# Kernel optimization log

Measured on AMD Instinct MI355X. Metric: run time of the kernel, lower is better.

Reference implementation:

```python
import jax, jax.numpy as jnp
import numpy as np

B, S, D = 2, 2048, 1024
H, DH, DL, DR = 16, 64, 512, 64
DHID, N_SHARED, N_ROUTED, TOPK = 512, 2, 8, 2
EPS = 1e-6


def setup_inputs() -> dict:
    key = jax.random.key(0)
    ks = jax.random.split(key, 16)
    w = lambda k, shp: jax.random.normal(k, shp, dtype=jnp.float32) * 0.02
    return {
        "x": jax.random.normal(ks[0], (B, S, D), dtype=jnp.float32),
        "mask": jnp.tril(jnp.ones((S, S), dtype=bool)),  # causal
        "w_q": w(ks[1], (D, H * (DH + DR))),
        "w_dkv": w(ks[2], (D, DL)),
        "w_uk": w(ks[3], (DL, H * DH)),
        "w_uv": w(ks[4], (DL, H * DH)),
        "w_kr": w(ks[5], (D, DR)),
        "w_o": w(ks[6], (H * DH, D)),
        "attn_norm_w": jnp.ones((D,), jnp.float32),
        "mlp_norm_w": jnp.ones((D,), jnp.float32),
        "gate_w": w(ks[7], (D, N_ROUTED)),
        "wr_gate": w(ks[8], (N_ROUTED, D, DHID)),
        "wr_up": w(ks[9], (N_ROUTED, D, DHID)),
        "wr_down": w(ks[10], (N_ROUTED, DHID, D)),
        "ws_gate": w(ks[11], (N_SHARED, D, DHID)),
        "ws_up": w(ks[12], (N_SHARED, D, DHID)),
        "ws_down": w(ks[13], (N_SHARED, DHID, D)),
    }


def _rmsnorm(x, w):
    x32 = x.astype(jnp.float32)
    n = x32 * jax.lax.rsqrt(jnp.mean(x32 * x32, axis=-1, keepdims=True) + EPS)
    return n.astype(x.dtype) * w


def _rope_tables(seq_len, dim):
    half = dim // 2
    inv = 1.0 / (10000.0 ** (jnp.arange(half, dtype=jnp.float32) / half))
    ang = jnp.arange(seq_len, dtype=jnp.float32)[:, None] * inv[None, :]  # [S, dim/2]
    return jnp.cos(ang), jnp.sin(ang)


def _rope(t, cos, sin):
    # t: [..., S, dim]; rotate-half convention
    t1, t2 = jnp.split(t, 2, axis=-1)
    return jnp.concatenate([t1 * cos - t2 * sin, t2 * cos + t1 * sin], axis=-1)


def _layer(x, mask, w_q, w_dkv, w_uk, w_uv, w_kr, w_o, attn_norm_w, mlp_norm_w,
           gate_w, wr_gate, wr_up, wr_down, ws_gate, ws_up, ws_down):
    # ---- pre-norm MLA attention + residual ----
    h = _rmsnorm(x, attn_norm_w)
    cos, sin = _rope_tables(S, DR)

    q = (h @ w_q).reshape(B, S, H, DH + DR).transpose(0, 2, 1, 3)  # [B,H,S,DH+DR]
    q_c, q_r = q[..., :DH], _rope(q[..., DH:], cos, sin)

    latent = h @ w_dkv                                              # [B,S,DL]
    k_c = (latent @ w_uk).reshape(B, S, H, DH).transpose(0, 2, 1, 3)  # [B,H,S,DH]
    v = (latent @ w_uv).reshape(B, S, H, DH).transpose(0, 2, 1, 3)
    k_r = _rope(h @ w_kr, cos, sin)                                 # [B,S,DR] shared across heads

    scale = 1.0 / np.sqrt(DH + DR)
    scores = (jnp.einsum("bhqd,bhkd->bhqk", q_c, k_c)
              + jnp.einsum("bhqd,bkd->bhqk", q_r, k_r)) * scale
    scores = jnp.where(mask, scores, jnp.float32(-1e9))
    attn = jax.nn.softmax(scores, axis=-1)
    ctx = jnp.einsum("bhqk,bhkd->bhqd", attn, v)                    # [B,H,S,DH]
    attn_out = ctx.transpose(0, 2, 1, 3).reshape(B, S, H * DH) @ w_o
    x = x + attn_out

    # ---- pre-norm shared + routed MoE FFN + residual ----
    h = _rmsnorm(x, mlp_norm_w).reshape(-1, D)                      # [T,D]
    probs = jax.nn.softmax(h @ gate_w, axis=-1)                     # [T,NR]
    vals, idx = jax.lax.top_k(probs, TOPK)                          # [T,K]
    gw = vals / jnp.sum(vals, axis=-1, keepdims=True)
    dense_w = jnp.sum(jax.nn.one_hot(idx, N_ROUTED, dtype=h.dtype) * gw[..., None], axis=1)  # [T,NR]

    g = jax.nn.silu(jnp.einsum("td,edh->teh", h, wr_gate))
    u = jnp.einsum("td,edh->teh", h, wr_up)
    y = jnp.einsum("teh,ehd->ted", g * u, wr_down)                  # [T,NR,D]
    routed = jnp.einsum("ted,te->td", y, dense_w)

    gs = jax.nn.silu(jnp.einsum("td,sdh->tsh", h, ws_gate))
    us = jnp.einsum("td,sdh->tsh", h, ws_up)
    shared = jnp.einsum("tsh,shd->td", gs * us, ws_down)

    return x + (routed + shared).reshape(B, S, D)


def reference(x, mask, w_q, w_dkv, w_uk, w_uv, w_kr, w_o, attn_norm_w, mlp_norm_w,
              gate_w, wr_gate, wr_up, wr_down, ws_gate, ws_up, ws_down):
    return _layer(x, mask, w_q, w_dkv, w_uk, w_uv, w_kr, w_o, attn_norm_w, mlp_norm_w,
                  gate_w, wr_gate, wr_up, wr_down, ws_gate, ws_up, ws_down)
```

## Files before the change

kernel.cpp:

```cpp
#include <hip/hip_runtime.h>
#include <hip/hip_bf16.h>
#include <stdint.h>

typedef unsigned short u16;
typedef __attribute__((ext_vector_type(8))) short short8;
typedef __attribute__((ext_vector_type(4))) float f32x4;
typedef __attribute__((ext_vector_type(4))) int i32x4;
typedef __attribute__((ext_vector_type(2))) unsigned int u32x2;

#define B_    2
#define S_    2048
#define D_    1024
#define H_    16
#define T_    (B_*S_)

static __device__ __forceinline__ float b2f(u16 h) { return __uint_as_float(((uint32_t)h) << 16); }
static __device__ __forceinline__ u16 f2b(float f) {
    uint32_t u = __float_as_uint(f);
    u += 0x7fffu + ((u >> 16) & 1u);
    return (u16)(u >> 16);
}
static __device__ __forceinline__ uint32_t pack2(float a, float b) {
    return (uint32_t)f2b(a) | ((uint32_t)f2b(b) << 16);
}
static __device__ __forceinline__ uint32_t cvtpk(float a, float b) {
    uint32_t r;
    asm("v_cvt_pk_bf16_f32 %0, %1, %2" : "=v"(r) : "v"(a), "v"(b));
    return r;
}
#define MFMA(a,b,c) __builtin_amdgcn_mfma_f32_16x16x32_bf16(a,b,c,0,0,0)

static __device__ __forceinline__ void gl2lds16(const void* g, void* l) {
    __builtin_amdgcn_global_load_lds((const __attribute__((address_space(1))) void*)g,
                                     (__attribute__((address_space(3))) void*)l, 16, 0, 0);
}

__global__ __launch_bounds__(256) void transpose_cvt(const float* __restrict__ in,
    u16* __restrict__ out, int K, int N, long inEZ, long outEZ)
{
    __shared__ float tile[32][33];
    const int e = blockIdx.z;
    const float* ip = in + (long)e * inEZ;
    u16* op = out + (long)e * outEZ;
    int n0 = blockIdx.x * 32, k0 = blockIdx.y * 32;
    int tx = threadIdx.x, ty = threadIdx.y;
#pragma unroll
    for (int i = 0; i < 4; ++i) {
        int k = k0 + ty + 8 * i, n = n0 + tx;
        tile[ty + 8 * i][tx] = (k < K && n < N) ? ip[(long)k * N + n] : 0.f;
    }
    __syncthreads();
#pragma unroll
    for (int i = 0; i < 4; ++i) {
        int n = n0 + ty + 8 * i, k = k0 + tx;
        if (n < N && k < K) op[(long)n * K + k] = f2b(tile[tx][ty + 8 * i]);
    }
}

__global__ __launch_bounds__(256) void gemm_k(const u16* __restrict__ A, long lda,
    const u16* __restrict__ Bt, long ldb, void* __restrict__ Cv, long ldc, int K,
    int mode, const float* __restrict__ resid)
{
    __shared__ u16 As[128 * 32];
    __shared__ u16 Bs[128 * 32];
    const int tid = threadIdx.x, lane = tid & 63, wave = tid >> 6;
    const int wm = (wave & 1) * 64, wn = (wave >> 1) * 64;
    const int quad = lane >> 4, rr = lane & 15, q8 = quad * 8;
    const long row0 = (long)blockIdx.y * 128, col0 = (long)blockIdx.x * 128;
    f32x4 acc[4][4];
#pragma unroll
    for (int i = 0; i < 4; ++i)
#pragma unroll
        for (int j = 0; j < 4; ++j)
#pragma unroll
            for (int c = 0; c < 4; ++c) acc[i][j][c] = 0.f;
    const int band = wave * 32;
    const u16* ga = A + (row0 + band + (lane >> 2)) * lda + (lane & 3) * 8;
    const u16* gb = Bt + (col0 + band + (lane >> 2)) * ldb + (lane & 3) * 8;
    u16* la = &As[band * 32];
    u16* lb = &Bs[band * 32];
    for (int k0 = 0; k0 < K; k0 += 32) {
        gl2lds16(ga + k0, la);
        gl2lds16(ga + k0 + 16 * lda, la + 16 * 32);
        gl2lds16(gb + k0, lb);
        gl2lds16(gb + k0 + 16 * ldb, lb + 16 * 32);
        __syncthreads();
        short8 af[4], bf[4];
#pragma unroll
        for (int mi = 0; mi < 4; ++mi) af[mi] = *(const short8*)&As[(wm + mi * 16 + rr) * 32 + q8];
#pragma unroll
        for (int ni = 0; ni < 4; ++ni) bf[ni] = *(const short8*)&Bs[(wn + ni * 16 + rr) * 32 + q8];
#pragma unroll
        for (int mi = 0; mi < 4; ++mi)
#pragma unroll
            for (int ni = 0; ni < 4; ++ni)
                acc[mi][ni] = MFMA(af[mi], bf[ni], acc[mi][ni]);
        __syncthreads();
    }
#pragma unroll
    for (int mi = 0; mi < 4; ++mi)
#pragma unroll
        for (int ni = 0; ni < 4; ++ni)
#pragma unroll
            for (int rg = 0; rg < 4; ++rg) {
                long r = row0 + wm + mi * 16 + quad * 4 + rg;
                long c = col0 + wn + ni * 16 + rr;
                float v = acc[mi][ni][rg];
                if (mode == 1)      ((u16*)Cv)[r * ldc + c] = f2b(v);
                else if (mode == 2) ((float*)Cv)[r * ldc + c] += v;
                else                ((float*)Cv)[r * ldc + c] = v + resid[r * 1024 + c];
            }
}

__global__ __launch_bounds__(256) void gemm_shdown(const u16* __restrict__ A,
    const u16* __restrict__ BtBase, float* __restrict__ Cv)
{
    __shared__ u16 As[128 * 32];
    __shared__ u16 Bs[128 * 32];
    const int tid = threadIdx.x, lane = tid & 63, wave = tid >> 6;
    const int wm = (wave & 1) * 64, wn = (wave >> 1) * 64;
    const int quad = lane >> 4, rr = lane & 15, q8 = quad * 8;
    const long row0 = (long)blockIdx.y * 128, col0 = (long)blockIdx.x * 128;
    f32x4 acc[4][4];
#pragma unroll
    for (int i = 0; i < 4; ++i)
#pragma unroll
        for (int j = 0; j < 4; ++j)
#pragma unroll
            for (int c = 0; c < 4; ++c) acc[i][j][c] = 0.f;
    const int band = wave * 32;
    const long arow = row0 + band + (lane >> 2);
    const long brow = col0 + band + (lane >> 2);
    u16* la = &As[band * 32];
    u16* lb = &Bs[band * 32];
    for (int k0 = 0; k0 < 1024; k0 += 32) {
        const long aoff = (k0 < 512) ? (long)k0 : (long)(512 + k0);
        const long boff = (k0 < 512) ? (long)k0 : (long)(524288 - 512 + k0);
        const u16* ga = A + arow * 2048 + aoff + (lane & 3) * 8;
        const u16* gb = BtBase + brow * 512 + boff + (lane & 3) * 8;
        gl2lds16(ga, la);
        gl2lds16(ga + 16 * 2048, la + 16 * 32);
        gl2lds16(gb, lb);
        gl2lds16(gb + 16 * 512, lb + 16 * 32);
        __syncthreads();
        short8 af[4], bf[4];
#pragma unroll
        for (int mi = 0; mi < 4; ++mi) af[mi] = *(const short8*)&As[(wm + mi * 16 + rr) * 32 + q8];
#pragma unroll
        for (int ni = 0; ni < 4; ++ni) bf[ni] = *(const short8*)&Bs[(wn + ni * 16 + rr) * 32 + q8];
#pragma unroll
        for (int mi = 0; mi < 4; ++mi)
#pragma unroll
            for (int ni = 0; ni < 4; ++ni)
                acc[mi][ni] = MFMA(af[mi], bf[ni], acc[mi][ni]);
        __syncthreads();
    }
#pragma unroll
    for (int mi = 0; mi < 4; ++mi)
#pragma unroll
        for (int ni = 0; ni < 4; ++ni)
#pragma unroll
            for (int rg = 0; rg < 4; ++rg) {
                long r = row0 + wm + mi * 16 + quad * 4 + rg;
                long c = col0 + wn + ni * 16 + rr;
                Cv[r * 1024 + c] += acc[mi][ni][rg];
            }
}

__global__ __launch_bounds__(256) void gemm_gather(const u16* __restrict__ H2,
    const u16* __restrict__ BtAll, u16* __restrict__ C,
    const int* __restrict__ cnt, const int* __restrict__ off,
    const int* __restrict__ elist)
{
    const int e = blockIdx.z;
    const int cntE = cnt[e], offE = off[e];
    const int m0 = blockIdx.y * 128;
    if (m0 >= cntE) return;
    const u16* Bt = BtAll + (long)e * 1024 * 1024;
    __shared__ u16 As[128 * 32];
    __shared__ u16 Bs[128 * 32];
    const int tid = threadIdx.x, lane = tid & 63, wave = tid >> 6;
    const int wm = (wave & 1) * 64, wn = (wave >> 1) * 64;
    const int quad = lane >> 4, rr = lane & 15, q8 = quad * 8;
    const long col0 = (long)blockIdx.x * 128;
    f32x4 acc[4][4];
#pragma unroll
    for (int i = 0; i < 4; ++i)
#pragma unroll
        for (int j = 0; j < 4; ++j)
#pragma unroll
            for (int c = 0; c < 4; ++c) acc[i][j][c] = 0.f;
    const int band = wave * 32;
    int r0 = m0 + band + (lane >> 2);
    int r1 = r0 + 16;
    int tok0 = elist[offE + (r0 < cntE ? r0 : cntE - 1)];
    int tok1 = elist[offE + (r1 < cntE ? r1 : cntE - 1)];
    const u16* ga0 = H2 + (long)tok0 * 1024 + (lane & 3) * 8;
    const u16* ga1 = H2 + (long)tok1 * 1024 + (lane & 3) * 8;
    const u16* gb = Bt + (col0 + band + (lane >> 2)) * 1024L + (lane & 3) * 8;
    u16* la = &As[band * 32];
    u16* lb = &Bs[band * 32];
    for (int k0 = 0; k0 < 1024; k0 += 32) {
        gl2lds16(ga0 + k0, la);
        gl2lds16(ga1 + k0, la + 16 * 32);
        gl2lds16(gb + k0, lb);
        gl2lds16(gb + k0 + 16 * 1024, lb + 16 * 32);
        __syncthreads();
        short8 af[4], bf[4];
#pragma unroll
        for (int mi = 0; mi < 4; ++mi) af[mi] = *(const short8*)&As[(wm + mi * 16 + rr) * 32 + q8];
#pragma unroll
        for (int ni = 0; ni < 4; ++ni) bf[ni] = *(const short8*)&Bs[(wn + ni * 16 + rr) * 32 + q8];
#pragma unroll
        for (int mi = 0; mi < 4; ++mi)
#pragma unroll
            for (int ni = 0; ni < 4; ++ni)
                acc[mi][ni] = MFMA(af[mi], bf[ni], acc[mi][ni]);
        __syncthreads();
    }
#pragma unroll
    for (int mi = 0; mi < 4; ++mi)
#pragma unroll
        for (int ni = 0; ni < 4; ++ni)
#pragma unroll
            for (int rg = 0; rg < 4; ++rg) {
                int ml = wm + mi * 16 + quad * 4 + rg;
                long c = col0 + wn + ni * 16 + rr;
                if (m0 + ml < cntE)
                    C[(long)(offE + m0 + ml) * 1024 + c] = f2b(acc[mi][ni][rg]);
            }
}

__global__ __launch_bounds__(256) void gemm_slot(const u16* __restrict__ Act,
    const u16* __restrict__ BtAll, u16* __restrict__ rout,
    const int* __restrict__ cnt, const int* __restrict__ off)
{
    const int e = blockIdx.z;
    const int cntE = cnt[e], offE = off[e];
    const int m0 = blockIdx.y * 128;
    if (m0 >= cntE) return;
    const u16* Bt = BtAll + (long)e * 1024 * 512;
    __shared__ u16 As[128 * 32];
    __shared__ u16 Bs[128 * 32];
    const int tid = threadIdx.x, lane = tid & 63, wave = tid >> 6;
    const int wm = (wave & 1) * 64, wn = (wave >> 1) * 64;
    const int quad = lane >> 4, rr = lane & 15, q8 = quad * 8;
    const long col0 = (long)blockIdx.x * 128;
    f32x4 acc[4][4];
#pragma unroll
    for (int i = 0; i < 4; ++i)
#pragma unroll
        for (int j = 0; j < 4; ++j)
#pragma unroll
            for (int c = 0; c < 4; ++c) acc[i][j][c] = 0.f;
    const int band = wave * 32;
    int r0 = offE + m0 + band + (lane >> 2); if (r0 > 8191) r0 = 8191;
    int r1 = r0 + 16; if (r1 > 8191) r1 = 8191;
    const u16* ga0 = Act + (long)r0 * 1024 + (lane & 3) * 8;
    const u16* ga1 = Act + (long)r1 * 1024 + (lane & 3) * 8;
    const u16* gb = Bt + (col0 + band + (lane >> 2)) * 512L + (lane & 3) * 8;
    u16* la = &As[band * 32];
    u16* lb = &Bs[band * 32];
    for (int k0 = 0; k0 < 512; k0 += 32) {
        gl2lds16(ga0 + k0, la);
        gl2lds16(ga1 + k0, la + 16 * 32);
        gl2lds16(gb + k0, lb);
        gl2lds16(gb + k0 + 16 * 512, lb + 16 * 32);
        __syncthreads();
        short8 af[4], bf[4];
#pragma unroll
        for (int mi = 0; mi < 4; ++mi) af[mi] = *(const short8*)&As[(wm + mi * 16 + rr) * 32 + q8];
#pragma unroll
        for (int ni = 0; ni < 4; ++ni) bf[ni] = *(const short8*)&Bs[(wn + ni * 16 + rr) * 32 + q8];
#pragma unroll
        for (int mi = 0; mi < 4; ++mi)
#pragma unroll
            for (int ni = 0; ni < 4; ++ni)
                acc[mi][ni] = MFMA(af[mi], bf[ni], acc[mi][ni]);
        __syncthreads();
    }
#pragma unroll
    for (int mi = 0; mi < 4; ++mi)
#pragma unroll
        for (int ni = 0; ni < 4; ++ni)
#pragma unroll
            for (int rg = 0; rg < 4; ++rg) {
                int ml = wm + mi * 16 + quad * 4 + rg;
                long c = col0 + wn + ni * 16 + rr;
                if (m0 + ml < cntE)
                    rout[(long)(offE + m0 + ml) * 1024 + c] = f2b(acc[mi][ni][rg]);
            }
}

__global__ __launch_bounds__(256) void rmsnorm_wave(const float* __restrict__ x,
    const float* __restrict__ w, u16* __restrict__ out)
{
    const int t = blockIdx.x * 4 + (threadIdx.x >> 6);
    const int lane = threadIdx.x & 63;
    const float* xp = x + (size_t)t * D_;
    f32x4 v[4];
    float s = 0.f;
#pragma unroll
    for (int i = 0; i < 4; ++i) {
        v[i] = *(const f32x4*)&xp[lane * 4 + i * 256];
#pragma unroll
        for (int j = 0; j < 4; ++j) s += v[i][j] * v[i][j];
    }
#pragma unroll
    for (int o = 32; o > 0; o >>= 1) s += __shfl_xor(s, o);
    const float inv = rsqrtf(s * (1.f / D_) + 1e-6f);
    u16* op = out + (size_t)t * D_;
#pragma unroll
    for (int i = 0; i < 4; ++i) {
        const int d = lane * 4 + i * 256;
        f32x4 wv = *(const f32x4*)&w[d];
        u32x2 pk;
        pk[0] = pack2(v[i][0] * inv * wv[0], v[i][1] * inv * wv[1]);
        pk[1] = pack2(v[i][2] * inv * wv[2], v[i][3] * inv * wv[3]);
        *(u32x2*)&op[d] = pk;
    }
}

__global__ __launch_bounds__(256) void rmsnorm_gate_fused(const float* __restrict__ xm,
    const float* __restrict__ nw, const float* __restrict__ gw, u16* __restrict__ h2,
    int* __restrict__ tok_e, float* __restrict__ tok_w)
{
    const int t = blockIdx.x * 4 + (threadIdx.x >> 6);
    const int lane = threadIdx.x & 63;
    const float* xp = xm + (size_t)t * D_;
    f32x4 v[4];
    float s = 0.f;
#pragma unroll
    for (int i = 0; i < 4; ++i) {
        v[i] = *(const f32x4*)&xp[lane * 4 + i * 256];
#pragma unroll
        for (int j = 0; j < 4; ++j) s += v[i][j] * v[i][j];
    }
#pragma unroll
    for (int o = 32; o > 0; o >>= 1) s += __shfl_xor(s, o);
    const float inv = rsqrtf(s * (1.f / D_) + 1e-6f);
    u16* op = h2 + (size_t)t * D_;
    float part[8] = {0,0,0,0,0,0,0,0};
#pragma unroll
    for (int i = 0; i < 4; ++i) {
        const int d = lane * 4 + i * 256;
        f32x4 wv = *(const f32x4*)&nw[d];
        float hv[4];
#pragma unroll
        for (int j = 0; j < 4; ++j) hv[j] = v[i][j] * inv * wv[j];
        u32x2 pk;
        pk[0] = pack2(hv[0], hv[1]);
        pk[1] = pack2(hv[2], hv[3]);
        *(u32x2*)&op[d] = pk;
#pragma unroll
        for (int j = 0; j < 4; ++j) {
            const float* gp = gw + (size_t)(d + j) * 8;
#pragma unroll
            for (int e = 0; e < 8; ++e) part[e] += hv[j] * gp[e];
        }
    }
#pragma unroll
    for (int e = 0; e < 8; ++e)
#pragma unroll
        for (int o = 32; o > 0; o >>= 1) part[e] += __shfl_xor(part[e], o);
    if (lane == 0) {
        float mx = part[0];
#pragma unroll
        for (int e = 1; e < 8; ++e) mx = fmaxf(mx, part[e]);
        float p[8];
#pragma unroll
        for (int e = 0; e < 8; ++e) p[e] = __expf(part[e] - mx);
        int i0 = 0;
#pragma unroll
        for (int e = 1; e < 8; ++e) if (p[e] > p[i0]) i0 = e;
        int i1 = (i0 == 0) ? 1 : 0;
#pragma unroll
        for (int e = 0; e < 8; ++e) { if (e == i0) continue; if (p[e] > p[i1]) i1 = e; }
        float sw = p[i0] + p[i1];
        tok_e[2 * t] = i0;  tok_e[2 * t + 1] = i1;
        tok_w[2 * t] = p[i0] / sw;  tok_w[2 * t + 1] = p[i1] / sw;
    }
}

__global__ __launch_bounds__(256) void moe_route(const int* __restrict__ tok_e,
    int* __restrict__ cnt, int* __restrict__ off,
    int* __restrict__ elist, int* __restrict__ tslot)
{
    const int E = blockIdx.x;
    const int tid = threadIdx.x, lane = tid & 63, wave = tid >> 6;
    int ev[32];
#pragma unroll
    for (int i = 0; i < 8; ++i)
        *(i32x4*)&ev[i * 4] = *(const i32x4*)&tok_e[tid * 32 + i * 4];
    int c8[8] = {0,0,0,0,0,0,0,0};
#pragma unroll
    for (int k = 0; k < 32; ++k) ++c8[ev[k] & 7];
    int incl[8];
#pragma unroll
    for (int e = 0; e < 8; ++e) {
        int vv = c8[e];
#pragma unroll
        for (int d = 1; d < 64; d <<= 1) {
            int tmp = __shfl_up(vv, d);
            if (lane >= d) vv += tmp;
        }
        incl[e] = vv;
    }
    __shared__ int wtot[4][8];
    if (lane == 63)
#pragma unroll
        for (int e = 0; e < 8; ++e) wtot[wave][e] = incl[e];
    __syncthreads();
    int tot[8];
#pragma unroll
    for (int e = 0; e < 8; ++e) tot[e] = wtot[0][e] + wtot[1][e] + wtot[2][e] + wtot[3][e];
    int waveoff = 0;
    for (int w = 0; w < 4; ++w) if (w < wave) waveoff += wtot[w][E];
    int offE = 0;
#pragma unroll
    for (int e = 0; e < 8; ++e) if (e < E) offE += tot[e];
    int rank = offE + waveoff + (incl[E] - c8[E]);
#pragma unroll
    for (int k = 0; k < 32; ++k) {
        if ((ev[k] & 7) == E) {
            int p = tid * 32 + k;
            elist[rank] = p >> 1;
            tslot[p] = rank;
            ++rank;
        }
    }
    if (tid == 0) { cnt[E] = tot[E]; off[E] = offE; }
}

__global__ __launch_bounds__(256) void rope_all(u16* __restrict__ proj)
{
    int idx = blockIdx.x * 256 + threadIdx.x;
    int i = idx & 31;
    int r = idx >> 5;
    int t = r / 17, which = r - t * 17;
    int s = t & (S_ - 1);
    float inv = __expf(-(float)i * 0.28782313662425575f);
    float ang = (float)s * inv;
    float c = cosf(ang), sn = sinf(ang);
    u16* base = proj + (size_t)t * 2688 + (which < 16 ? which * 128 + 64 : 2560);
    float t1 = b2f(base[i]), t2 = b2f(base[32 + i]);
    base[i]      = f2b(t1 * c - t2 * sn);
    base[32 + i] = f2b(t2 * c + t1 * sn);
}

__global__ __launch_bounds__(256, 4) void attn_flash(const u16* __restrict__ proj,
    const u16* __restrict__ kc, const u16* __restrict__ vt, u16* __restrict__ ctx)
{
    const int qidx = blockIdx.x >> 5;
    const int qt = (qidx < 8) ? (31 - qidx) : (qidx < 16) ? (qidx - 8)
                 : (qidx < 24) ? (39 - qidx) : (qidx - 16);
    const int bh = blockIdx.x & 31;
    const int b = bh >> 4, h = bh & 15;
    const int q0 = qt * 64;
    const int tid = threadIdx.x, lane = tid & 63, wave = tid >> 6;
    const int quad = lane >> 4, rr = lane & 15, q8 = quad * 8;
    const int wm2 = wave * 16;

    __shared__ u16 Ks[64 * 128];
    __shared__ u16 Ps[64 * 64];

    const long tbase = (long)b * S_ + q0;
    short8 qf[4];
#pragma unroll
    for (int d0 = 0; d0 < 4; ++d0)
        qf[d0] = *(const short8*)&proj[(tbase + wm2 + rr) * 2688 + h * 128 + d0 * 32 + q8];

    f32x4 accO[4];
    float m_i = -3e38f, l_i = 0.f;
#pragma unroll
    for (int vi = 0; vi < 4; ++vi)
#pragma unroll
        for (int rg = 0; rg < 4; ++rg) accO[vi][rg] = 0.f;
    const float sc = 0.08838834764831845f * 1.4426950408889634f;

    const int srow0 = tid >> 3, sg = tid & 7;
    const int swz = sg ^ (srow0 & 7);
    const u16* kcp = kc   + ((long)b * S_ + srow0) * 1024 + h * 64 + sg * 8;
    const u16* krp = proj + ((long)b * S_ + srow0) * 2688 + 2560 + sg * 8;
    const u16* vbase = vt + (size_t)(h * 64 + rr) * 4096 + b * 2048 + q8;
    const int rg7 = rr & 7;
    int rdcol[4];
#pragma unroll
    for (int d0 = 0; d0 < 4; ++d0) rdcol[d0] = ((d0 * 4 + quad) ^ rg7) * 8;
    const int pwcol0 = ((quad * 8) ^ (rg7 << 3));
    const int prcol0 = (((quad * 16) ^ (rg7 << 4)) >> 1);
    const int prcol1 = (((64 + quad * 16) ^ (rg7 << 4)) >> 1);

    const int nkt = qt + 1;
    short8 rk0 = *(const short8*)(kcp);
    short8 rk1 = *(const short8*)(kcp + 32 * 1024);
    short8 rm0 = *(const short8*)(krp);
    short8 rm1 = *(const short8*)(krp + (size_t)32 * 2688);

    for (int kt = 0; kt < nkt; ++kt) {
        const int k0 = kt * 64;
        *(short8*)&Ks[srow0 * 128 + swz * 8]             = rk0;
        *(short8*)&Ks[(srow0 + 32) * 128 + swz * 8]      = rk1;
        *(short8*)&Ks[srow0 * 128 + 64 + swz * 8]        = rm0;
        *(short8*)&Ks[(srow0 + 32) * 128 + 64 + swz * 8] = rm1;
        __syncthreads();

        const size_t k0s = (kt + 1 < nkt) ? (size_t)(k0 + 64) : 0;
        short8 nk0 = *(const short8*)(kcp + k0s * 1024);
        short8 nk1 = *(const short8*)(kcp + k0s * 1024 + 32 * 1024);
        short8 nm0 = *(const short8*)(krp + k0s * 2688);
        short8 nm1 = *(const short8*)(krp + k0s * 2688 + (size_t)32 * 2688);

        f32x4 accS[4];
#pragma unroll
        for (int ki = 0; ki < 4; ++ki)
#pragma unroll
            for (int rg = 0; rg < 4; ++rg) accS[ki][rg] = 0.f;
        __builtin_amdgcn_s_setprio(1);
#pragma unroll
        for (int d0 = 0; d0 < 4; ++d0) {
            short8 kf[4];
#pragma unroll
            for (int ki = 0; ki < 4; ++ki) kf[ki] = *(const short8*)&Ks[(ki * 16 + rr) * 128 + rdcol[d0]];
#pragma unroll
            for (int ki = 0; ki < 4; ++ki) accS[ki] = MFMA(kf[ki], qf[d0], accS[ki]);
        }
        __builtin_amdgcn_s_setprio(0);
        __syncthreads();

        short8 vf0[4], vf1[4];
#pragma unroll
        for (int vi = 0; vi < 4; ++vi) {
            vf0[vi] = *(const short8*)(vbase + (size_t)vi * 16 * 4096 + k0);
            vf1[vi] = *(const short8*)(vbase + (size_t)vi * 16 * 4096 + k0 + 32);
        }

        float mx = -3e38f;
        if (kt == qt) {
            const int qg = q0 + wm2 + rr;
#pragma unroll
            for (int ki = 0; ki < 4; ++ki)
#pragma unroll
                for (int rg = 0; rg < 4; ++rg) {
                    float w = accS[ki][rg] * sc;
                    if (k0 + ki * 16 + quad * 4 + rg > qg) w = -1e30f;
                    accS[ki][rg] = w;
                    mx = fmaxf(mx, w);
                }
        } else {
#pragma unroll
            for (int ki = 0; ki < 4; ++ki)
#pragma unroll
                for (int rg = 0; rg < 4; ++rg) {
                    float w = accS[ki][rg] * sc;
                    accS[ki][rg] = w;
                    mx = fmaxf(mx, w);
                }
        }
        mx = fmaxf(mx, __shfl_xor(mx, 16));
        mx = fmaxf(mx, __shfl_xor(mx, 32));
        if (__any(mx > m_i)) {
            float mnew = fmaxf(m_i, mx);
            float alpha = exp2f(m_i - mnew);
            m_i = mnew;
            l_i *= alpha;
#pragma unroll
            for (int vi = 0; vi < 4; ++vi)
#pragma unroll
                for (int rg = 0; rg < 4; ++rg) accO[vi][rg] *= alpha;
        }
        float ps = 0.f;
#pragma unroll
        for (int ki = 0; ki < 4; ++ki) {
            float p0 = exp2f(accS[ki][0] - m_i);
            float p1 = exp2f(accS[ki][1] - m_i);
            float p2 = exp2f(accS[ki][2] - m_i);
            float p3 = exp2f(accS[ki][3] - m_i);
            ps += (p0 + p1) + (p2 + p3);
            u32x2 pk; pk[0] = cvtpk(p0, p1); pk[1] = cvtpk(p2, p3);
            *(u32x2*)&Ps[(wm2 + rr) * 64 + ((((ki * 32 + quad * 8) ^ (rg7 << 4)) >> 1))] = pk;
        }
        ps += __shfl_xor(ps, 16);
        ps += __shfl_xor(ps, 32);
        l_i += ps;

        short8 pf0 = *(const short8*)&Ps[(wm2 + rr) * 64 + prcol0];
        short8 pf1 = *(const short8*)&Ps[(wm2 + rr) * 64 + prcol1];
        __builtin_amdgcn_s_setprio(1);
#pragma unroll
        for (int vi = 0; vi < 4; ++vi) accO[vi] = MFMA(vf0[vi], pf0, accO[vi]);
#pragma unroll
        for (int vi = 0; vi < 4; ++vi) accO[vi] = MFMA(vf1[vi], pf1, accO[vi]);
        __builtin_amdgcn_s_setprio(0);

        rk0 = nk0; rk1 = nk1; rm0 = nm0; rm1 = nm1;
    }
    {
        float linv = 1.f / l_i;
        long t = tbase + wm2 + rr;
#pragma unroll
        for (int vi = 0; vi < 4; ++vi) {
            u32x2 pk;
            pk[0] = pack2(accO[vi][0] * linv, accO[vi][1] * linv);
            pk[1] = pack2(accO[vi][2] * linv, accO[vi][3] * linv);
            *(u32x2*)&ctx[t * 1024 + h * 64 + vi * 16 + quad * 4] = pk;
        }
    }
    (void)pwcol0;
}

__global__ __launch_bounds__(256) void silu_mul(u16* __restrict__ gu, int nPairRows)
{
    int i = blockIdx.x * 256 + threadIdx.x;
    if (i >= nPairRows * 64) return;
    int row = i >> 6, j8 = (i & 63) * 8;
    long base = (long)row * 1024;
    short8 g8 = *(const short8*)&gu[base + j8];
    short8 u8 = *(const short8*)&gu[base + 512 + j8];
    short8 r;
#pragma unroll
    for (int j = 0; j < 8; ++j) {
        float g = b2f((u16)g8[j]), u = b2f((u16)u8[j]);
        r[j] = (short)f2b(g / (1.f + __expf(-g)) * u);
    }
    *(short8*)&gu[base + j8] = r;
}

__global__ __launch_bounds__(256) void final_kernel(const float* __restrict__ xm,
    const u16* __restrict__ rout, const int* __restrict__ tok_slot,
    const float* __restrict__ tok_w, float* __restrict__ out)
{
    long i = ((long)blockIdx.x * 256 + threadIdx.x) * 4;
    int t = (int)(i >> 10), d = (int)(i & 1023);
    int s0 = tok_slot[2 * t], s1 = tok_slot[2 * t + 1];
    float w0 = tok_w[2 * t], w1 = tok_w[2 * t + 1];
    f32x4 xv = *(const f32x4*)&xm[i];
    u32x2 r0 = *(const u32x2*)&rout[(long)s0 * 1024 + d];
    u32x2 r1 = *(const u32x2*)&rout[(long)s1 * 1024 + d];
    f32x4 o;
    o[0] = xv[0] + w0 * b2f((u16)(r0[0] & 0xffffu)) + w1 * b2f((u16)(r1[0] & 0xffffu));
    o[1] = xv[1] + w0 * b2f((u16)(r0[0] >> 16))     + w1 * b2f((u16)(r1[0] >> 16));
    o[2] = xv[2] + w0 * b2f((u16)(r0[1] & 0xffffu)) + w1 * b2f((u16)(r1[1] & 0xffffu));
    o[3] = xv[3] + w0 * b2f((u16)(r0[1] >> 16))     + w1 * b2f((u16)(r1[1] >> 16));
    *(f32x4*)&out[i] = o;
}

#define OFF_XMID   0UL
#define OFF_H      16777216UL
#define OFF_PROJ   25165824UL
#define OFF_WGU    25165824UL
#define OFF_KC     47185920UL
#define OFF_WD     47185920UL
#define OFF_VT     55574528UL
#define OFF_GUR    57671680UL
#define OFF_CTX    63963136UL
#define OFF_WATT   72351744UL
#define OFF_ROUT   74448896UL
#define OFF_GUS    91226112UL
#define OFF_TOKE   108003328UL
#define OFF_TOKW   108036096UL
#define OFF_TSLOT  108068864UL
#define OFF_ELIST  108101632UL
#define OFF_META   108134400UL

extern "C" void kernel_launch(void* const* d_in, const int* in_sizes, int n_in,
                              void* d_out, int out_size, void* d_ws, size_t ws_size,
                              hipStream_t stream)
{
    const float* x       = (const float*)d_in[0];
    const float* w_q     = (const float*)d_in[2];
    const float* w_dkv   = (const float*)d_in[3];
    const float* w_uk    = (const float*)d_in[4];
    const float* w_uv    = (const float*)d_in[5];
    const float* w_kr    = (const float*)d_in[6];
    const float* w_o     = (const float*)d_in[7];
    const float* attn_nw = (const float*)d_in[8];
    const float* mlp_nw  = (const float*)d_in[9];
    const float* gate_w  = (const float*)d_in[10];
    const float* wr_gate = (const float*)d_in[11];
    const float* wr_up   = (const float*)d_in[12];
    const float* wr_down = (const float*)d_in[13];
    const float* ws_gate = (const float*)d_in[14];
    const float* ws_up   = (const float*)d_in[15];
    const float* ws_down = (const float*)d_in[16];
    float* out = (float*)d_out;

    char* W = (char*)d_ws;
    float* x_mid = (float*)(W + OFF_XMID);
    u16* h      = (u16*)(W + OFF_H);
    u16* h2     = (u16*)(W + OFF_H);
    u16* proj   = (u16*)(W + OFF_PROJ);
    u16* wgu_t  = (u16*)(W + OFF_WGU);
    u16* kc     = (u16*)(W + OFF_KC);
    u16* wd_t   = (u16*)(W + OFF_WD);
    u16* vt     = (u16*)(W + OFF_VT);
    u16* gu_r   = (u16*)(W + OFF_GUR);
    u16* ctx    = (u16*)(W + OFF_CTX);
    u16* wqkv_t = (u16*)(W + OFF_WATT);
    u16* wuk_t  = wqkv_t + 2688 * 1024;
    u16* wuv_t  = wuk_t + 1024 * 512;
    u16* wo_t   = wuv_t + 1024 * 512;
    u16* rout   = (u16*)(W + OFF_ROUT);
    u16* gu_s   = (u16*)(W + OFF_GUS);
    int*   tok_e = (int*)(W + OFF_TOKE);
    float* tok_w = (float*)(W + OFF_TOKW);
    int*   tslot = (int*)(W + OFF_TSLOT);
    int*   elist = (int*)(W + OFF_ELIST);
    int*   meta  = (int*)(W + OFF_META);
    int* cnt = meta, * off = meta + 8;

    dim3 tb(32, 8);
    transpose_cvt<<<dim3(64, 32, 1), tb, 0, stream>>>(w_q,   wqkv_t,               1024, 2048, 0, 0);
    transpose_cvt<<<dim3(16, 32, 1), tb, 0, stream>>>(w_dkv, wqkv_t + 2048 * 1024, 1024, 512,  0, 0);
    transpose_cvt<<<dim3(2,  32, 1), tb, 0, stream>>>(w_kr,  wqkv_t + 2560 * 1024, 1024, 64,   0, 0);
    transpose_cvt<<<dim3(32, 16, 1), tb, 0, stream>>>(w_uk,  wuk_t,                512,  1024, 0, 0);
    transpose_cvt<<<dim3(32, 16, 1), tb, 0, stream>>>(w_uv,  wuv_t,                512,  1024, 0, 0);
    transpose_cvt<<<dim3(32, 32, 1), tb, 0, stream>>>(w_o,   wo_t,                 1024, 1024, 0, 0);

    rmsnorm_wave<<<T_ / 4, 256, 0, stream>>>(x, attn_nw, h);
    gemm_k<<<dim3(21, 32), 256, 0, stream>>>(h, 1024, wqkv_t, 1024, proj, 2688, 1024, 1, nullptr);
    rope_all<<<(T_ * 17 * 32) / 256, 256, 0, stream>>>(proj);
    gemm_k<<<dim3(8, 32), 256, 0, stream>>>(proj + 2048, 2688, wuk_t, 512, kc, 1024, 512, 1, nullptr);
    gemm_k<<<dim3(32, 8), 256, 0, stream>>>(wuv_t, 512, proj + 2048, 2688, vt, 4096, 512, 1, nullptr);
    attn_flash<<<1024, 256, 0, stream>>>(proj, kc, vt, ctx);
    gemm_k<<<dim3(8, 32), 256, 0, stream>>>(ctx, 1024, wo_t, 1024, x_mid, 1024, 1024, 3, x);

    transpose_cvt<<<dim3(16, 32, 8), tb, 0, stream>>>(wr_gate, wgu_t,              1024, 512, 524288, 1048576);
    transpose_cvt<<<dim3(16, 32, 8), tb, 0, stream>>>(wr_up,   wgu_t + 512 * 1024, 1024, 512, 524288, 1048576);
    transpose_cvt<<<dim3(16, 32, 2), tb, 0, stream>>>(ws_gate, wgu_t + 8 * 1048576,              1024, 512, 524288, 1048576);
    transpose_cvt<<<dim3(16, 32, 2), tb, 0, stream>>>(ws_up,   wgu_t + 8 * 1048576 + 512 * 1024, 1024, 512, 524288, 1048576);
    transpose_cvt<<<dim3(32, 16, 8), tb, 0, stream>>>(wr_down, wd_t,               512, 1024, 524288, 524288);
    transpose_cvt<<<dim3(32, 16, 2), tb, 0, stream>>>(ws_down, wd_t + 8 * 524288,  512, 1024, 524288, 524288);

    rmsnorm_gate_fused<<<T_ / 4, 256, 0, stream>>>(x_mid, mlp_nw, gate_w, h2, tok_e, tok_w);
    moe_route<<<8, 256, 0, stream>>>(tok_e, cnt, off, elist, tslot);
    gemm_gather<<<dim3(8, 64, 8), 256, 0, stream>>>(h2, wgu_t, gu_r, cnt, off, elist);
    silu_mul<<<(8192 * 64) / 256, 256, 0, stream>>>(gu_r, 8192);
    gemm_slot<<<dim3(8, 64, 8), 256, 0, stream>>>(gu_r, wd_t, rout, cnt, off);
    gemm_k<<<dim3(16, 32), 256, 0, stream>>>(h2, 1024, wgu_t + 8 * 1048576, 1024, gu_s, 2048, 1024, 1, nullptr);
    silu_mul<<<(8192 * 64) / 256, 256, 0, stream>>>(gu_s, 8192);
    gemm_shdown<<<dim3(8, 32), 256, 0, stream>>>(gu_s, wd_t + 8 * 524288, x_mid);
    final_kernel<<<(T_ * D_) / 1024, 256, 0, stream>>>(x_mid, rout, tslot, tok_w, out);
}
```

Baseline: 580.8 us.

## Triple-buffer LDS in all GEMM kernels with async prefetch two tiles ahead

Each of the four GEMM kernels now keeps three LDS stages for A and B and issues the global-to-LDS loads for tile t+2 while computing tile t. Explicit vmcnt waits plus a single barrier per iteration replace the two __syncthreads per tile of the old single-buffer loop. This aims to hide global memory latency behind MFMA work. In exchange LDS use per block triples to 48KB, which may lower occupancy. An unused variable in the attention kernel is also removed.

```diff
diff --git a/kernel.cpp b/kernel.cpp
--- a/kernel.cpp
+++ b/kernel.cpp
@@ -61,8 +61,8 @@
     const u16* __restrict__ Bt, long ldb, void* __restrict__ Cv, long ldc, int K,
     int mode, const float* __restrict__ resid)
 {
-    __shared__ u16 As[128 * 32];
-    __shared__ u16 Bs[128 * 32];
+    __shared__ u16 As[3][128 * 32];
+    __shared__ u16 Bs[3][128 * 32];
     const int tid = threadIdx.x, lane = tid & 63, wave = tid >> 6;
     const int wm = (wave & 1) * 64, wn = (wave >> 1) * 64;
     const int quad = lane >> 4, rr = lane & 15, q8 = quad * 8;
@@ -77,26 +77,38 @@
     const int band = wave * 32;
     const u16* ga = A + (row0 + band + (lane >> 2)) * lda + (lane & 3) * 8;
     const u16* gb = Bt + (col0 + band + (lane >> 2)) * ldb + (lane & 3) * 8;
-    u16* la = &As[band * 32];
-    u16* lb = &Bs[band * 32];
-    for (int k0 = 0; k0 < K; k0 += 32) {
-        gl2lds16(ga + k0, la);
-        gl2lds16(ga + k0 + 16 * lda, la + 16 * 32);
-        gl2lds16(gb + k0, lb);
-        gl2lds16(gb + k0 + 16 * ldb, lb + 16 * 32);
-        __syncthreads();
+    const int lo = band * 32;
+    const int nt = K >> 5;
+#define STG(bi, k0s) do { \
+    gl2lds16(ga + (k0s), &As[bi][lo]); \
+    gl2lds16(ga + (k0s) + 16 * lda, &As[bi][lo + 512]); \
+    gl2lds16(gb + (k0s), &Bs[bi][lo]); \
+    gl2lds16(gb + (k0s) + 16 * ldb, &Bs[bi][lo + 512]); } while (0)
+    STG(0, 0);
+    STG(1, 32);
+    asm volatile("s_waitcnt vmcnt(4)" ::: "memory");
+    __builtin_amdgcn_s_barrier();
+    int cur = 0, nx2 = 2;
+    for (int t = 0; t < nt; ++t) {
+        const bool more = (t + 2 < nt);
+        if (more) STG(nx2, (t + 2) * 32);
         short8 af[4], bf[4];
 #pragma unroll
-        for (int mi = 0; mi < 4; ++mi) af[mi] = *(const short8*)&As[(wm + mi * 16 + rr) * 32 + q8];
-#pragma unroll
-        for (int ni = 0; ni < 4; ++ni) bf[ni] = *(const short8*)&Bs[(wn + ni * 16 + rr) * 32 + q8];
+        for (int mi = 0; mi < 4; ++mi) af[mi] = *(const short8*)&As[cur][(wm + mi * 16 + rr) * 32 + q8];
+#pragma unroll
+        for (int ni = 0; ni < 4; ++ni) bf[ni] = *(const short8*)&Bs[cur][(wn + ni * 16 + rr) * 32 + q8];
 #pragma unroll
         for (int mi = 0; mi < 4; ++mi)
 #pragma unroll
             for (int ni = 0; ni < 4; ++ni)
                 acc[mi][ni] = MFMA(af[mi], bf[ni], acc[mi][ni]);
-        __syncthreads();
-    }
+        if (more) asm volatile("s_waitcnt vmcnt(4)" ::: "memory");
+        else      asm volatile("s_waitcnt vmcnt(0)" ::: "memory");
+        __builtin_amdgcn_s_barrier();
+        cur = (cur == 2) ? 0 : cur + 1;
+        nx2 = (nx2 == 2) ? 0 : nx2 + 1;
+    }
+#undef STG
 #pragma unroll
     for (int mi = 0; mi < 4; ++mi)
 #pragma unroll
@@ -115,8 +127,8 @@
 __global__ __launch_bounds__(256) void gemm_shdown(const u16* __restrict__ A,
     const u16* __restrict__ BtBase, float* __restrict__ Cv)
 {
-    __shared__ u16 As[128 * 32];
-    __shared__ u16 Bs[128 * 32];
+    __shared__ u16 As[3][128 * 32];
+    __shared__ u16 Bs[3][128 * 32];
     const int tid = threadIdx.x, lane = tid & 63, wave = tid >> 6;
     const int wm = (wave & 1) * 64, wn = (wave >> 1) * 64;
     const int quad = lane >> 4, rr = lane & 15, q8 = quad * 8;
@@ -131,30 +143,42 @@
     const int band = wave * 32;
     const long arow = row0 + band + (lane >> 2);
     const long brow = col0 + band + (lane >> 2);
-    u16* la = &As[band * 32];
-    u16* lb = &Bs[band * 32];
-    for (int k0 = 0; k0 < 1024; k0 += 32) {
-        const long aoff = (k0 < 512) ? (long)k0 : (long)(512 + k0);
-        const long boff = (k0 < 512) ? (long)k0 : (long)(524288 - 512 + k0);
-        const u16* ga = A + arow * 2048 + aoff + (lane & 3) * 8;
-        const u16* gb = BtBase + brow * 512 + boff + (lane & 3) * 8;
-        gl2lds16(ga, la);
-        gl2lds16(ga + 16 * 2048, la + 16 * 32);
-        gl2lds16(gb, lb);
-        gl2lds16(gb + 16 * 512, lb + 16 * 32);
-        __syncthreads();
+    const int lo = band * 32;
+#define STG(bi, k0s) do { \
+    const long aoff = ((k0s) < 512) ? (long)(k0s) : (long)(512 + (k0s)); \
+    const long boff = ((k0s) < 512) ? (long)(k0s) : (long)(524288 - 512 + (k0s)); \
+    const u16* ga = A + arow * 2048 + aoff + (lane & 3) * 8; \
+    const u16* gb = BtBase + brow * 512 + boff + (lane & 3) * 8; \
+    gl2lds16(ga, &As[bi][lo]); \
+    gl2lds16(ga + 16 * 2048, &As[bi][lo + 512]); \
+    gl2lds16(gb, &Bs[bi][lo]); \
+    gl2lds16(gb + 16 * 512, &Bs[bi][lo + 512]); } while (0)
+    const int nt = 32;
+    STG(0, 0);
+    STG(1, 32);
+    asm volatile("s_waitcnt vmcnt(4)" ::: "memory");
+    __builtin_amdgcn_s_barrier();
+    int cur = 0, nx2 = 2;
+    for (int t = 0; t < nt; ++t) {
+        const bool more = (t + 2 < nt);
+        if (more) STG(nx2, (t + 2) * 32);
         short8 af[4], bf[4];
 #pragma unroll
-        for (int mi = 0; mi < 4; ++mi) af[mi] = *(const short8*)&As[(wm + mi * 16 + rr) * 32 + q8];
-#pragma unroll
-        for (int ni = 0; ni < 4; ++ni) bf[ni] = *(const short8*)&Bs[(wn + ni * 16 + rr) * 32 + q8];
+        for (int mi = 0; mi < 4; ++mi) af[mi] = *(const short8*)&As[cur][(wm + mi * 16 + rr) * 32 + q8];
+#pragma unroll
+        for (int ni = 0; ni < 4; ++ni) bf[ni] = *(const short8*)&Bs[cur][(wn + ni * 16 + rr) * 32 + q8];
 #pragma unroll
         for (int mi = 0; mi < 4; ++mi)
 #pragma unroll
             for (int ni = 0; ni < 4; ++ni)
                 acc[mi][ni] = MFMA(af[mi], bf[ni], acc[mi][ni]);
-        __syncthreads();
-    }
+        if (more) asm volatile("s_waitcnt vmcnt(4)" ::: "memory");
+        else      asm volatile("s_waitcnt vmcnt(0)" ::: "memory");
+        __builtin_amdgcn_s_barrier();
+        cur = (cur == 2) ? 0 : cur + 1;
+        nx2 = (nx2 == 2) ? 0 : nx2 + 1;
+    }
+#undef STG
 #pragma unroll
     for (int mi = 0; mi < 4; ++mi)
 #pragma unroll
@@ -177,8 +201,8 @@
     const int m0 = blockIdx.y * 128;
     if (m0 >= cntE) return;
     const u16* Bt = BtAll + (long)e * 1024 * 1024;
-    __shared__ u16 As[128 * 32];
-    __shared__ u16 Bs[128 * 32];
+    __shared__ u16 As[3][128 * 32];
+    __shared__ u16 Bs[3][128 * 32];
     const int tid = threadIdx.x, lane = tid & 63, wave = tid >> 6;
     const int wm = (wave & 1) * 64, wn = (wave >> 1) * 64;
     const int quad = lane >> 4, rr = lane & 15, q8 = quad * 8;
@@ -198,26 +222,38 @@
     const u16* ga0 = H2 + (long)tok0 * 1024 + (lane & 3) * 8;
     const u16* ga1 = H2 + (long)tok1 * 1024 + (lane & 3) * 8;
     const u16* gb = Bt + (col0 + band + (lane >> 2)) * 1024L + (lane & 3) * 8;
-    u16* la = &As[band * 32];
-    u16* lb = &Bs[band * 32];
-    for (int k0 = 0; k0 < 1024; k0 += 32) {
-        gl2lds16(ga0 + k0, la);
-        gl2lds16(ga1 + k0, la + 16 * 32);
-        gl2lds16(gb + k0, lb);
-        gl2lds16(gb + k0 + 16 * 1024, lb + 16 * 32);
-        __syncthreads();
+    const int lo = band * 32;
+#define STG(bi, k0s) do { \
+    gl2lds16(ga0 + (k0s), &As[bi][lo]); \
+    gl2lds16(ga1 + (k0s), &As[bi][lo + 512]); \
+    gl2lds16(gb + (k0s), &Bs[bi][lo]); \
+    gl2lds16(gb + (k0s) + 16 * 1024, &Bs[bi][lo + 512]); } while (0)
+    const int nt = 32;
+    STG(0, 0);
+    STG(1, 32);
+    asm volatile("s_waitcnt vmcnt(4)" ::: "memory");
+    __builtin_amdgcn_s_barrier();
+    int cur = 0, nx2 = 2;
+    for (int t = 0; t < nt; ++t) {
+        const bool more = (t + 2 < nt);
+        if (more) STG(nx2, (t + 2) * 32);
         short8 af[4], bf[4];
 #pragma unroll
-        for (int mi = 0; mi < 4; ++mi) af[mi] = *(const short8*)&As[(wm + mi * 16 + rr) * 32 + q8];
-#pragma unroll
-        for (int ni = 0; ni < 4; ++ni) bf[ni] = *(const short8*)&Bs[(wn + ni * 16 + rr) * 32 + q8];
+        for (int mi = 0; mi < 4; ++mi) af[mi] = *(const short8*)&As[cur][(wm + mi * 16 + rr) * 32 + q8];
+#pragma unroll
+        for (int ni = 0; ni < 4; ++ni) bf[ni] = *(const short8*)&Bs[cur][(wn + ni * 16 + rr) * 32 + q8];
 #pragma unroll
         for (int mi = 0; mi < 4; ++mi)
 #pragma unroll
             for (int ni = 0; ni < 4; ++ni)
                 acc[mi][ni] = MFMA(af[mi], bf[ni], acc[mi][ni]);
-        __syncthreads();
-    }
+        if (more) asm volatile("s_waitcnt vmcnt(4)" ::: "memory");
+        else      asm volatile("s_waitcnt vmcnt(0)" ::: "memory");
+        __builtin_amdgcn_s_barrier();
+        cur = (cur == 2) ? 0 : cur + 1;
+        nx2 = (nx2 == 2) ? 0 : nx2 + 1;
+    }
+#undef STG
 #pragma unroll
     for (int mi = 0; mi < 4; ++mi)
 #pragma unroll
@@ -240,8 +276,8 @@
     const int m0 = blockIdx.y * 128;
     if (m0 >= cntE) return;
     const u16* Bt = BtAll + (long)e * 1024 * 512;
-    __shared__ u16 As[128 * 32];
-    __shared__ u16 Bs[128 * 32];
+    __shared__ u16 As[3][128 * 32];
+    __shared__ u16 Bs[3][128 * 32];
     const int tid = threadIdx.x, lane = tid & 63, wave = tid >> 6;
     const int wm = (wave & 1) * 64, wn = (wave >> 1) * 64;
     const int quad = lane >> 4, rr = lane & 15, q8 = quad * 8;
@@ -259,26 +295,38 @@
     const u16* ga0 = Act + (long)r0 * 1024 + (lane & 3) * 8;
     const u16* ga1 = Act + (long)r1 * 1024 + (lane & 3) * 8;
     const u16* gb = Bt + (col0 + band + (lane >> 2)) * 512L + (lane & 3) * 8;
-    u16* la = &As[band * 32];
-    u16* lb = &Bs[band * 32];
-    for (int k0 = 0; k0 < 512; k0 += 32) {
-        gl2lds16(ga0 + k0, la);
-        gl2lds16(ga1 + k0, la + 16 * 32);
-        gl2lds16(gb + k0, lb);
-        gl2lds16(gb + k0 + 16 * 512, lb + 16 * 32);
-        __syncthreads();
+    const int lo = band * 32;
+#define STG(bi, k0s) do { \
+    gl2lds16(ga0 + (k0s), &As[bi][lo]); \
+    gl2lds16(ga1 + (k0s), &As[bi][lo + 512]); \
+    gl2lds16(gb + (k0s), &Bs[bi][lo]); \
+    gl2lds16(gb + (k0s) + 16 * 512, &Bs[bi][lo + 512]); } while (0)
+    const int nt = 16;
+    STG(0, 0);
+    STG(1, 32);
+    asm volatile("s_waitcnt vmcnt(4)" ::: "memory");
+    __builtin_amdgcn_s_barrier();
+    int cur = 0, nx2 = 2;
+    for (int t = 0; t < nt; ++t) {
+        const bool more = (t + 2 < nt);
+        if (more) STG(nx2, (t + 2) * 32);
         short8 af[4], bf[4];
 #pragma unroll
-        for (int mi = 0; mi < 4; ++mi) af[mi] = *(const short8*)&As[(wm + mi * 16 + rr) * 32 + q8];
-#pragma unroll
-        for (int ni = 0; ni < 4; ++ni) bf[ni] = *(const short8*)&Bs[(wn + ni * 16 + rr) * 32 + q8];
+        for (int mi = 0; mi < 4; ++mi) af[mi] = *(const short8*)&As[cur][(wm + mi * 16 + rr) * 32 + q8];
+#pragma unroll
+        for (int ni = 0; ni < 4; ++ni) bf[ni] = *(const short8*)&Bs[cur][(wn + ni * 16 + rr) * 32 + q8];
 #pragma unroll
         for (int mi = 0; mi < 4; ++mi)
 #pragma unroll
             for (int ni = 0; ni < 4; ++ni)
                 acc[mi][ni] = MFMA(af[mi], bf[ni], acc[mi][ni]);
-        __syncthreads();
-    }
+        if (more) asm volatile("s_waitcnt vmcnt(4)" ::: "memory");
+        else      asm volatile("s_waitcnt vmcnt(0)" ::: "memory");
+        __builtin_amdgcn_s_barrier();
+        cur = (cur == 2) ? 0 : cur + 1;
+        nx2 = (nx2 == 2) ? 0 : nx2 + 1;
+    }
+#undef STG
 #pragma unroll
     for (int mi = 0; mi < 4; ++mi)
 #pragma unroll
@@ -487,7 +535,6 @@
     int rdcol[4];
 #pragma unroll
     for (int d0 = 0; d0 < 4; ++d0) rdcol[d0] = ((d0 * 4 + quad) ^ rg7) * 8;
-    const int pwcol0 = ((quad * 8) ^ (rg7 << 3));
     const int prcol0 = (((quad * 16) ^ (rg7 << 4)) >> 1);
     const int prcol1 = (((64 + quad * 16) ^ (rg7 << 4)) >> 1);
 
@@ -606,7 +653,6 @@
             *(u32x2*)&ctx[t * 1024 + h * 64 + vi * 16 + quad * 4] = pk;
         }
     }
-    (void)pwcol0;
 }
 
 __global__ __launch_bounds__(256) void silu_mul(u16* __restrict__ gu, int nPairRows)
```

Result: no change. 570.8 us (-1.7%).
